# Kernel tuning notes

Measured on AMD Instinct MI355X. Metric: run time of the kernel, lower is better.

Reference implementation:

```python
import jax, jax.numpy as jnp
import numpy as np

B, S, E = 4, 2048, 1024
H = 16
D = E // H  # head_size = 64


def setup_inputs() -> dict:
    key = jax.random.key(0)
    k1, k2, k3 = jax.random.split(key, 3)
    scale = 0.02
    return {
        "x": jax.random.normal(k1, (B, S, E), dtype=jnp.float32),
        "w_qkv": jax.random.normal(k2, (E, 3 * E), dtype=jnp.float32) * scale,
        "b_qkv": jnp.zeros((3 * E,), dtype=jnp.float32),
        "w_proj": jax.random.normal(k3, (E, E), dtype=jnp.float32) * scale,
        "b_proj": jnp.zeros((E,), dtype=jnp.float32),
    }


def reference(x, w_qkv, b_qkv, w_proj, b_proj):
    bsz, seq_len, embd = x.shape
    qkv = x @ w_qkv + b_qkv                              # [B,S,3E]
    q, k, v = jnp.split(qkv, 3, axis=2)
    # [B,S,E] -> [B,H,S,D]
    q = q.reshape(bsz, seq_len, H, D).transpose(0, 2, 1, 3)
    k = k.reshape(bsz, seq_len, H, D).transpose(0, 2, 1, 3)
    v = v.reshape(bsz, seq_len, H, D).transpose(0, 2, 1, 3)
    att = jnp.einsum("bhqd,bhkd->bhqk", q, k) / jnp.sqrt(jnp.float32(D))
    causal = jnp.tril(jnp.ones((seq_len, seq_len), dtype=bool))
    att = jnp.where(causal[None, None, :, :], att, -jnp.inf)
    att = jax.nn.softmax(att, axis=-1)
    y = jnp.einsum("bhqk,bhkd->bhqd", att, v)            # [B,H,S,D]
    y = y.transpose(0, 2, 1, 3).reshape(bsz, seq_len, embd)
    return y @ w_proj + b_proj
```

## Files before the change

kernel.cpp:

```cpp
#include <hip/hip_runtime.h>
#include <cmath>
#include <cstdint>

#define BB 4
#define SS 2048
#define EE 1024
#define HH 16
#define DD 64
#define ROWS (BB*SS)
#define QKV_N (3*EE)

using bf16x8 = __attribute__((ext_vector_type(8))) __bf16;
using bf16x4 = __attribute__((ext_vector_type(4))) __bf16;
using f32x4  = __attribute__((ext_vector_type(4))) float;

__device__ inline f32x4 mfma16(bf16x8 a, bf16x8 b, f32x4 c) {
    return __builtin_amdgcn_mfma_f32_16x16x32_bf16(a, b, c, 0, 0, 0);
}

__device__ inline void load_lds16(const void* g, void* l) {
    __builtin_amdgcn_global_load_lds(
        (__attribute__((address_space(1))) void*)g,
        (__attribute__((address_space(3))) void*)l, 16, 0, 0);
}

__global__ __launch_bounds__(256) void cast_f32_bf16(const float* __restrict__ in,
                                                     __bf16* __restrict__ out) {
    size_t i = ((size_t)blockIdx.x * 256 + threadIdx.x) * 4;
    float4 v = *(const float4*)(in + i);
    bf16x4 o;
    o[0] = (__bf16)v.x; o[1] = (__bf16)v.y; o[2] = (__bf16)v.z; o[3] = (__bf16)v.w;
    *(bf16x4*)(out + i) = o;
}

__global__ __launch_bounds__(256) void transpose_cast(const float* __restrict__ in,
                                                      __bf16* __restrict__ out,
                                                      int K, int N) {
    __shared__ float tile[32][33];
    int n0 = blockIdx.x * 32, k0 = blockIdx.y * 32;
    int tx = threadIdx.x, ty = threadIdx.y;
#pragma unroll
    for (int i = 0; i < 4; ++i)
        tile[ty + 8 * i][tx] = in[(size_t)(k0 + ty + 8 * i) * N + n0 + tx];
    __syncthreads();
#pragma unroll
    for (int i = 0; i < 4; ++i)
        out[(size_t)(n0 + ty + 8 * i) * K + k0 + tx] = (__bf16)tile[tx][ty + 8 * i];
}

__global__ __launch_bounds__(256) void build_vt(const __bf16* __restrict__ qkv,
                                                __bf16* __restrict__ vt) {
    __shared__ __bf16 tile[64 * 72];
    const int s0 = blockIdx.x * 64, h = blockIdx.y, b = blockIdx.z;
    const int tid = threadIdx.x;
#pragma unroll
    for (int r = 0; r < 2; ++r) {
        int c = r * 256 + tid;
        int s = c >> 3, dp = c & 7;
        bf16x8 v = *(const bf16x8*)(qkv + (size_t)(b * SS + s0 + s) * QKV_N + 2048 + h * 64 + dp * 8);
        *(bf16x8*)(tile + s * 72 + dp * 8) = v;
    }
    __syncthreads();
#pragma unroll
    for (int r = 0; r < 2; ++r) {
        int c = r * 256 + tid;
        int d = c >> 3, sp = c & 7;
        bf16x8 o;
#pragma unroll
        for (int i = 0; i < 8; ++i) o[i] = tile[(sp * 8 + i) * 72 + d];
        *(bf16x8*)(vt + (size_t)((b * HH + h) * 64 + d) * SS + s0 + sp * 8) = o;
    }
}

template <bool OUT_BF16>
__global__ __launch_bounds__(256) void gemm_bt(const __bf16* __restrict__ A,
                                               const __bf16* __restrict__ Bt,
                                               const float* __restrict__ bias,
                                               void* __restrict__ Cout,
                                               int M, int N, int K) {
    __shared__ __bf16 As[128 * 32];
    __shared__ __bf16 Bs[128 * 32];
    const int tid  = threadIdx.x;
    const int wave = tid >> 6;
    const int lane = tid & 63;
    const int lrow = lane & 15;
    const int quad = lane >> 4;
    const int wm   = (wave >> 1) * 64;
    const int wn   = (wave & 1) * 64;
    const int tm   = blockIdx.x * 128;
    const int tn   = blockIdx.y * 128;

    f32x4 acc[4][4] = {};

    const int srow = lane >> 2;
    const int skoff = (lane & 3) * 8;

    for (int k0 = 0; k0 < K; k0 += 32) {
        __syncthreads();
#pragma unroll
        for (int i = 0; i < 2; ++i) {
            int c = wave * 2 + i;
            int row = 16 * c + srow;
            load_lds16(A + (size_t)(tm + row) * K + k0 + skoff, As + c * 512);
            load_lds16(Bt + (size_t)(tn + row) * K + k0 + skoff, Bs + c * 512);
        }
        __syncthreads();

        bf16x8 bfr[4];
#pragma unroll
        for (int ni = 0; ni < 4; ++ni)
            bfr[ni] = *(const bf16x8*)(Bs + (wn + ni * 16 + lrow) * 32 + quad * 8);
#pragma unroll
        for (int mi = 0; mi < 4; ++mi) {
            bf16x8 a = *(const bf16x8*)(As + (wm + mi * 16 + lrow) * 32 + quad * 8);
#pragma unroll
            for (int ni = 0; ni < 4; ++ni)
                acc[mi][ni] = mfma16(a, bfr[ni], acc[mi][ni]);
        }
    }

#pragma unroll
    for (int ni = 0; ni < 4; ++ni) {
        int cn = tn + wn + ni * 16 + lrow;
        float bv = bias[cn];
#pragma unroll
        for (int mi = 0; mi < 4; ++mi) {
#pragma unroll
            for (int r = 0; r < 4; ++r) {
                int gm = tm + wm + mi * 16 + quad * 4 + r;
                float v = acc[mi][ni][r] + bv;
                if (OUT_BF16)
                    ((__bf16*)Cout)[(size_t)gm * N + cn] = (__bf16)v;
                else
                    ((float*)Cout)[(size_t)gm * N + cn] = v;
            }
        }
    }
}

__global__ __launch_bounds__(256) void attn2(const __bf16* __restrict__ qkv,
                                             const __bf16* __restrict__ vt,
                                             __bf16* __restrict__ y) {
    const int qt = gridDim.x - 1 - blockIdx.x;
    const int h = blockIdx.y, b = blockIdx.z;
    const int tid = threadIdx.x;
    const int wave = tid >> 6, lane = tid & 63;
    const int lrow = lane & 15, quad = lane >> 4;
    const int qbase = qt * 64;

    __shared__ __bf16 Klds[64 * 64];
    __shared__ __bf16 Vlds[64 * 64];
    __shared__ __bf16 Plds[4 * 16 * 72];
    __bf16* Pw = Plds + wave * 16 * 72;

    const int qg = qbase + wave * 16 + lrow;
    const __bf16* qp = qkv + (size_t)(b * SS + qg) * QKV_N + h * 64;
    bf16x8 qf0 = *(const bf16x8*)(qp + quad * 8);
    bf16x8 qf1 = *(const bf16x8*)(qp + 32 + quad * 8);

    float m2 = -INFINITY, l = 0.f;
    f32x4 oacc[4] = {};

    const int nkb = qt + 1;
    for (int kb_i = 0; kb_i < nkb; ++kb_i) {
        const int kb = kb_i * 64;
        __syncthreads();
#pragma unroll
        for (int r = 0; r < 2; ++r) {
            int c = r * 256 + tid;
            int row = c >> 3;
            int gg = (c & 7) ^ (row & 7);
            load_lds16(qkv + (size_t)(b * SS + kb + row) * QKV_N + 1024 + h * 64 + gg * 8,
                       Klds + c * 8);
            load_lds16(vt + (size_t)((b * HH + h) * 64 + row) * SS + kb + gg * 8,
                       Vlds + c * 8);
        }
        __syncthreads();

        f32x4 s[4];
#pragma unroll
        for (int t = 0; t < 4; ++t) {
            const __bf16* kr = Klds + (16 * t + lrow) * 64;
            bf16x8 kf0 = *(const bf16x8*)(kr + 8 * (quad ^ (lrow & 7)));
            bf16x8 kf1 = *(const bf16x8*)(kr + 8 * ((4 + quad) ^ (lrow & 7)));
            f32x4 a = {};
            a = mfma16(kf0, qf0, a);
            a = mfma16(kf1, qf1, a);
            s[t] = a;
        }

        const float sc = 0.18033688f;
        float mx = -INFINITY;
        if (kb_i == nkb - 1) {
#pragma unroll
            for (int t = 0; t < 4; ++t)
#pragma unroll
                for (int r = 0; r < 4; ++r) {
                    int key = kb + 16 * t + 4 * quad + r;
                    float v = (key <= qg) ? s[t][r] * sc : -INFINITY;
                    s[t][r] = v;
                    mx = fmaxf(mx, v);
                }
        } else {
#pragma unroll
            for (int t = 0; t < 4; ++t)
#pragma unroll
                for (int r = 0; r < 4; ++r) {
                    float v = s[t][r] * sc;
                    s[t][r] = v;
                    mx = fmaxf(mx, v);
                }
        }
        mx = fmaxf(mx, __shfl_xor(mx, 16));
        mx = fmaxf(mx, __shfl_xor(mx, 32));
        float mnew = fmaxf(m2, mx);
        float alpha = exp2f(m2 - mnew);
        m2 = mnew;
        float rs = 0.f;
#pragma unroll
        for (int t = 0; t < 4; ++t) {
            bf16x4 pk;
#pragma unroll
            for (int r = 0; r < 4; ++r) {
                float e = exp2f(s[t][r] - mnew);
                rs += e;
                pk[r] = (__bf16)e;
            }
            *(bf16x4*)(Pw + lrow * 72 + 16 * t + 4 * quad) = pk;
        }
        rs += __shfl_xor(rs, 16);
        rs += __shfl_xor(rs, 32);
        l = l * alpha + rs;
#pragma unroll
        for (int td = 0; td < 4; ++td) {
            oacc[td][0] *= alpha; oacc[td][1] *= alpha;
            oacc[td][2] *= alpha; oacc[td][3] *= alpha;
        }

#pragma unroll
        for (int kh = 0; kh < 2; ++kh) {
            bf16x8 pf = *(const bf16x8*)(Pw + lrow * 72 + 32 * kh + 8 * quad);
#pragma unroll
            for (int td = 0; td < 4; ++td) {
                bf16x8 vf = *(const bf16x8*)(Vlds + (16 * td + lrow) * 64 +
                                             8 * ((4 * kh + quad) ^ (lrow & 7)));
                oacc[td] = mfma16(vf, pf, oacc[td]);
            }
        }
    }

    float linv = 1.f / l;
    __bf16* yp = y + (size_t)(b * SS + qg) * EE + h * 64;
#pragma unroll
    for (int td = 0; td < 4; ++td) {
        bf16x4 o;
#pragma unroll
        for (int r = 0; r < 4; ++r) o[r] = (__bf16)(oacc[td][r] * linv);
        *(bf16x4*)(yp + 16 * td + 4 * quad) = o;
    }
}

extern "C" void kernel_launch(void* const* d_in, const int* in_sizes, int n_in,
                              void* d_out, int out_size, void* d_ws, size_t ws_size,
                              hipStream_t stream) {
    const float* x      = (const float*)d_in[0];
    const float* w_qkv  = (const float*)d_in[1];
    const float* b_qkv  = (const float*)d_in[2];
    const float* w_proj = (const float*)d_in[3];
    const float* b_proj = (const float*)d_in[4];
    float* out = (float*)d_out;

    __bf16* xb     = (__bf16*)d_ws;
    __bf16* wqkvT  = xb + (size_t)ROWS * EE;
    __bf16* wprojT = wqkvT + (size_t)QKV_N * EE;
    __bf16* qkv    = wprojT + (size_t)EE * EE;
    __bf16* yb     = qkv + (size_t)ROWS * QKV_N;
    __bf16* vtb    = xb;

    cast_f32_bf16<<<dim3(ROWS * EE / 1024), dim3(256), 0, stream>>>(x, xb);
    transpose_cast<<<dim3(QKV_N / 32, EE / 32), dim3(32, 8), 0, stream>>>(w_qkv, wqkvT, EE, QKV_N);
    transpose_cast<<<dim3(EE / 32, EE / 32), dim3(32, 8), 0, stream>>>(w_proj, wprojT, EE, EE);
    gemm_bt<true><<<dim3(ROWS / 128, QKV_N / 128), dim3(256), 0, stream>>>(
        xb, wqkvT, b_qkv, (void*)qkv, ROWS, QKV_N, EE);
    build_vt<<<dim3(SS / 64, HH, BB), dim3(256), 0, stream>>>(qkv, vtb);
    attn2<<<dim3(SS / 64, HH, BB), dim3(256), 0, stream>>>(qkv, vtb, yb);
    gemm_bt<false><<<dim3(ROWS / 128, EE / 128), dim3(256), 0, stream>>>(
        yb, wprojT, b_proj, (void*)out, ROWS, EE, EE);
}
```

Baseline: 366.0 us.

## Widen attention tiles to 128 queries/keys, keep P in registers, fold scale into QKV GEMM

The attention kernel now handles 128 queries per block as two 64-row groups and 128-key blocks. Each K/V tile loaded into LDS is therefore reused across twice as many queries. The softmax probabilities stay in registers and feed 16x16x16 bf16 MFMAs directly, which removes the LDS round trip for P. The softmax scale is applied to Q in the QKV GEMM epilogue. The cost is more registers and LDS per block (launch bounds set to 3 blocks), half as many blocks, and more wasted work on the diagonal causal tiles.

```diff
diff --git a/kernel.cpp b/kernel.cpp
--- a/kernel.cpp
+++ b/kernel.cpp
@@ -13,9 +13,30 @@
 using bf16x8 = __attribute__((ext_vector_type(8))) __bf16;
 using bf16x4 = __attribute__((ext_vector_type(4))) __bf16;
 using f32x4  = __attribute__((ext_vector_type(4))) float;
+typedef __attribute__((ext_vector_type(4))) short short4v;
+
+#define SCQ 0.18033688f
 
 __device__ inline f32x4 mfma16(bf16x8 a, bf16x8 b, f32x4 c) {
     return __builtin_amdgcn_mfma_f32_16x16x32_bf16(a, b, c, 0, 0, 0);
+}
+
+__device__ inline f32x4 mfma16k16(bf16x4 a, bf16x4 b, f32x4 c) {
+#if defined(__HIP_DEVICE_COMPILE__)
+#if __has_builtin(__builtin_amdgcn_mfma_f32_16x16x16bf16_1k)
+    return __builtin_amdgcn_mfma_f32_16x16x16bf16_1k(
+        __builtin_bit_cast(short4v, a), __builtin_bit_cast(short4v, b), c, 0, 0, 0);
+#else
+    f32x4 d;
+    asm volatile("v_mfma_f32_16x16x16_bf16 %0, %1, %2, %3\n\ts_nop 7\n\ts_nop 3"
+                 : "=v"(d)
+                 : "v"(__builtin_bit_cast(short4v, a)),
+                   "v"(__builtin_bit_cast(short4v, b)), "v"(c));
+    return d;
+#endif
+#else
+    return c;
+#endif
 }
 
 __device__ inline void load_lds16(const void* g, void* l) {
@@ -72,7 +93,7 @@
     }
 }
 
-template <bool OUT_BF16>
+template <bool OUT_BF16, bool QSCALE>
 __global__ __launch_bounds__(256) void gemm_bt(const __bf16* __restrict__ A,
                                                const __bf16* __restrict__ Bt,
                                                const float* __restrict__ bias,
@@ -123,12 +144,13 @@
     for (int ni = 0; ni < 4; ++ni) {
         int cn = tn + wn + ni * 16 + lrow;
         float bv = bias[cn];
+        float sc = (QSCALE && cn < EE) ? SCQ : 1.0f;
 #pragma unroll
         for (int mi = 0; mi < 4; ++mi) {
 #pragma unroll
             for (int r = 0; r < 4; ++r) {
                 int gm = tm + wm + mi * 16 + quad * 4 + r;
-                float v = acc[mi][ni][r] + bv;
+                float v = (acc[mi][ni][r] + bv) * sc;
                 if (OUT_BF16)
                     ((__bf16*)Cout)[(size_t)gm * N + cn] = (__bf16)v;
                 else
@@ -138,125 +160,141 @@
     }
 }
 
-__global__ __launch_bounds__(256) void attn2(const __bf16* __restrict__ qkv,
-                                             const __bf16* __restrict__ vt,
-                                             __bf16* __restrict__ y) {
+__global__ __launch_bounds__(256, 3) void attn3(const __bf16* __restrict__ qkv,
+                                                const __bf16* __restrict__ vt,
+                                                __bf16* __restrict__ y) {
     const int qt = gridDim.x - 1 - blockIdx.x;
     const int h = blockIdx.y, b = blockIdx.z;
     const int tid = threadIdx.x;
     const int wave = tid >> 6, lane = tid & 63;
     const int lrow = lane & 15, quad = lane >> 4;
-    const int qbase = qt * 64;
-
-    __shared__ __bf16 Klds[64 * 64];
-    __shared__ __bf16 Vlds[64 * 64];
-    __shared__ __bf16 Plds[4 * 16 * 72];
-    __bf16* Pw = Plds + wave * 16 * 72;
-
-    const int qg = qbase + wave * 16 + lrow;
-    const __bf16* qp = qkv + (size_t)(b * SS + qg) * QKV_N + h * 64;
-    bf16x8 qf0 = *(const bf16x8*)(qp + quad * 8);
-    bf16x8 qf1 = *(const bf16x8*)(qp + 32 + quad * 8);
-
-    float m2 = -INFINITY, l = 0.f;
-    f32x4 oacc[4] = {};
-
-    const int nkb = qt + 1;
-    for (int kb_i = 0; kb_i < nkb; ++kb_i) {
-        const int kb = kb_i * 64;
+    const int qbase = qt * 128;
+
+    __shared__ __bf16 Klds[128 * 64];
+    __shared__ __bf16 Vlds[64 * 128];
+
+    const __bf16* kbase = qkv + (size_t)b * SS * QKV_N + 1024 + h * 64;
+    const __bf16* vbase = vt + (size_t)(b * HH + h) * 64 * SS;
+
+    bf16x8 qf[2][2];
+#pragma unroll
+    for (int g = 0; g < 2; ++g) {
+        const __bf16* qp = qkv + (size_t)(b * SS + qbase + 64 * g + wave * 16 + lrow) * QKV_N + h * 64;
+        qf[g][0] = *(const bf16x8*)(qp + quad * 8);
+        qf[g][1] = *(const bf16x8*)(qp + 32 + quad * 8);
+    }
+    const int q0 = qbase + wave * 16 + lrow;
+
+    float m[2] = {-INFINITY, -INFINITY}, l[2] = {0.f, 0.f};
+    f32x4 oacc[2][4] = {};
+
+    for (int kb_i = 0; kb_i <= qt; ++kb_i) {
+        const int kb = kb_i * 128;
         __syncthreads();
 #pragma unroll
-        for (int r = 0; r < 2; ++r) {
+        for (int r = 0; r < 4; ++r) {
             int c = r * 256 + tid;
             int row = c >> 3;
-            int gg = (c & 7) ^ (row & 7);
-            load_lds16(qkv + (size_t)(b * SS + kb + row) * QKV_N + 1024 + h * 64 + gg * 8,
-                       Klds + c * 8);
-            load_lds16(vt + (size_t)((b * HH + h) * 64 + row) * SS + kb + gg * 8,
-                       Vlds + c * 8);
+            int g8 = ((c & 7) ^ (row & 7)) * 8;
+            load_lds16(kbase + (size_t)(kb + row) * QKV_N + g8, Klds + c * 8);
+        }
+#pragma unroll
+        for (int r = 0; r < 4; ++r) {
+            int c = r * 256 + tid;
+            int d = c >> 4, kc = c & 15;
+            int g8 = ((kc & 8) | ((kc & 7) ^ (d & 7))) * 8;
+            load_lds16(vbase + (size_t)d * SS + kb + g8, Vlds + c * 8);
         }
         __syncthreads();
 
-        f32x4 s[4];
-#pragma unroll
-        for (int t = 0; t < 4; ++t) {
+        f32x4 s0[8], s1[8];
+#pragma unroll
+        for (int t = 0; t < 8; ++t) {
             const __bf16* kr = Klds + (16 * t + lrow) * 64;
             bf16x8 kf0 = *(const bf16x8*)(kr + 8 * (quad ^ (lrow & 7)));
             bf16x8 kf1 = *(const bf16x8*)(kr + 8 * ((4 + quad) ^ (lrow & 7)));
             f32x4 a = {};
-            a = mfma16(kf0, qf0, a);
-            a = mfma16(kf1, qf1, a);
-            s[t] = a;
-        }
-
-        const float sc = 0.18033688f;
-        float mx = -INFINITY;
-        if (kb_i == nkb - 1) {
-#pragma unroll
-            for (int t = 0; t < 4; ++t)
+            a = mfma16(kf0, qf[0][0], a);
+            a = mfma16(kf1, qf[0][1], a);
+            s0[t] = a;
+            f32x4 c = {};
+            c = mfma16(kf0, qf[1][0], c);
+            c = mfma16(kf1, qf[1][1], c);
+            s1[t] = c;
+        }
+
+        if (kb_i == qt) {
+#pragma unroll
+            for (int t = 0; t < 8; ++t)
 #pragma unroll
                 for (int r = 0; r < 4; ++r) {
                     int key = kb + 16 * t + 4 * quad + r;
-                    float v = (key <= qg) ? s[t][r] * sc : -INFINITY;
-                    s[t][r] = v;
-                    mx = fmaxf(mx, v);
+                    if (key > q0)      s0[t][r] = -INFINITY;
+                    if (key > q0 + 64) s1[t][r] = -INFINITY;
                 }
-        } else {
-#pragma unroll
-            for (int t = 0; t < 4; ++t)
+        }
+
+        bf16x4 p0[8], p1[8];
+#pragma unroll
+        for (int g = 0; g < 2; ++g) {
+            f32x4* s = g ? s1 : s0;
+            bf16x4* p = g ? p1 : p0;
+            float mx = -INFINITY;
+#pragma unroll
+            for (int t = 0; t < 8; ++t) {
+                float a = fmaxf(fmaxf(s[t][0], s[t][1]), fmaxf(s[t][2], s[t][3]));
+                mx = fmaxf(mx, a);
+            }
+            mx = fmaxf(mx, __shfl_xor(mx, 16));
+            mx = fmaxf(mx, __shfl_xor(mx, 32));
+            float mnew = fmaxf(m[g], mx);
+            float alpha = exp2f(m[g] - mnew);
+            m[g] = mnew;
+            float rs = 0.f;
+#pragma unroll
+            for (int t = 0; t < 8; ++t) {
 #pragma unroll
                 for (int r = 0; r < 4; ++r) {
-                    float v = s[t][r] * sc;
-                    s[t][r] = v;
-                    mx = fmaxf(mx, v);
+                    float e = exp2f(s[t][r] - mnew);
+                    rs += e;
+                    p[t][r] = (__bf16)e;
                 }
-        }
-        mx = fmaxf(mx, __shfl_xor(mx, 16));
-        mx = fmaxf(mx, __shfl_xor(mx, 32));
-        float mnew = fmaxf(m2, mx);
-        float alpha = exp2f(m2 - mnew);
-        m2 = mnew;
-        float rs = 0.f;
-#pragma unroll
-        for (int t = 0; t < 4; ++t) {
-            bf16x4 pk;
-#pragma unroll
-            for (int r = 0; r < 4; ++r) {
-                float e = exp2f(s[t][r] - mnew);
-                rs += e;
-                pk[r] = (__bf16)e;
-            }
-            *(bf16x4*)(Pw + lrow * 72 + 16 * t + 4 * quad) = pk;
-        }
-        rs += __shfl_xor(rs, 16);
-        rs += __shfl_xor(rs, 32);
-        l = l * alpha + rs;
+            }
+            rs += __shfl_xor(rs, 16);
+            rs += __shfl_xor(rs, 32);
+            l[g] = l[g] * alpha + rs;
+#pragma unroll
+            for (int td = 0; td < 4; ++td) {
+                oacc[g][td][0] *= alpha; oacc[g][td][1] *= alpha;
+                oacc[g][td][2] *= alpha; oacc[g][td][3] *= alpha;
+            }
+        }
+
+#pragma unroll
+        for (int t = 0; t < 8; ++t) {
+            int klog = 2 * t + (quad >> 1);
+            int c = (klog & 8) | ((klog & 7) ^ (lrow & 7));
+            const __bf16* vcol = Vlds + (size_t)lrow * 128 + c * 8 + 4 * (quad & 1);
+#pragma unroll
+            for (int td = 0; td < 4; ++td) {
+                bf16x4 vf = *(const bf16x4*)(vcol + td * 16 * 128);
+                oacc[0][td] = mfma16k16(vf, p0[t], oacc[0][td]);
+                oacc[1][td] = mfma16k16(vf, p1[t], oacc[1][td]);
+            }
+        }
+    }
+
+#pragma unroll
+    for (int g = 0; g < 2; ++g) {
+        float linv = 1.f / l[g];
+        __bf16* yp = y + (size_t)(b * SS + qbase + 64 * g + wave * 16 + lrow) * EE + h * 64;
 #pragma unroll
         for (int td = 0; td < 4; ++td) {
-            oacc[td][0] *= alpha; oacc[td][1] *= alpha;
-            oacc[td][2] *= alpha; oacc[td][3] *= alpha;
-        }
-
-#pragma unroll
-        for (int kh = 0; kh < 2; ++kh) {
-            bf16x8 pf = *(const bf16x8*)(Pw + lrow * 72 + 32 * kh + 8 * quad);
-#pragma unroll
-            for (int td = 0; td < 4; ++td) {
-                bf16x8 vf = *(const bf16x8*)(Vlds + (16 * td + lrow) * 64 +
-                                             8 * ((4 * kh + quad) ^ (lrow & 7)));
-                oacc[td] = mfma16(vf, pf, oacc[td]);
-            }
-        }
-    }
-
-    float linv = 1.f / l;
-    __bf16* yp = y + (size_t)(b * SS + qg) * EE + h * 64;
-#pragma unroll
-    for (int td = 0; td < 4; ++td) {
-        bf16x4 o;
-#pragma unroll
-        for (int r = 0; r < 4; ++r) o[r] = (__bf16)(oacc[td][r] * linv);
-        *(bf16x4*)(yp + 16 * td + 4 * quad) = o;
+            bf16x4 o;
+#pragma unroll
+            for (int r = 0; r < 4; ++r) o[r] = (__bf16)(oacc[g][td][r] * linv);
+            *(bf16x4*)(yp + 16 * td + 4 * quad) = o;
+        }
     }
 }
 
@@ -280,10 +318,10 @@
     cast_f32_bf16<<<dim3(ROWS * EE / 1024), dim3(256), 0, stream>>>(x, xb);
     transpose_cast<<<dim3(QKV_N / 32, EE / 32), dim3(32, 8), 0, stream>>>(w_qkv, wqkvT, EE, QKV_N);
     transpose_cast<<<dim3(EE / 32, EE / 32), dim3(32, 8), 0, stream>>>(w_proj, wprojT, EE, EE);
-    gemm_bt<true><<<dim3(ROWS / 128, QKV_N / 128), dim3(256), 0, stream>>>(
+    gemm_bt<true, true><<<dim3(ROWS / 128, QKV_N / 128), dim3(256), 0, stream>>>(
         xb, wqkvT, b_qkv, (void*)qkv, ROWS, QKV_N, EE);
     build_vt<<<dim3(SS / 64, HH, BB), dim3(256), 0, stream>>>(qkv, vtb);
-    attn2<<<dim3(SS / 64, HH, BB), dim3(256), 0, stream>>>(qkv, vtb, yb);
-    gemm_bt<false><<<dim3(ROWS / 128, EE / 128), dim3(256), 0, stream>>>(
+    attn3<<<dim3(SS / 128, HH, BB), dim3(256), 0, stream>>>(qkv, vtb, yb);
+    gemm_bt<false, false><<<dim3(ROWS / 128, EE / 128), dim3(256), 0, stream>>>(
         yb, wprojT, b_proj, (void*)out, ROWS, EE, EE);
 }
```

Result: slower. 483.4 us (+32.1%).
